# Optimization experiments

Measured on AMD Instinct MI355X. Metric: run time of the kernel, lower is better.

## Reference

```python
import jax, jax.numpy as jnp
import numpy as np

B, T, M, P = 128, 256, 256, 256  # batch, time, encoder dim m, decoder LSTM dim p


def setup_inputs() -> dict:
    key = jax.random.key(0)
    ks = jax.random.split(key, 10)
    init = lambda k, shape: (jax.random.normal(k, shape, jnp.float32) * 0.05)
    return {
        "data": jax.random.normal(ks[0], (B, T - 1, 1), jnp.float32),
        "enc_h": jax.random.normal(ks[1], (B, T, M), jnp.float32),
        "h0": jnp.zeros((B, P), jnp.float32),
        "c0": jnp.zeros((B, P), jnp.float32),
        # Dense(1) on concat([x_t, context]) -> input dim 1 + M
        "Wd": init(ks[2], (1 + M, 1)), "bd": jnp.zeros((1,), jnp.float32),
        # LSTM(p): kernel (in=1, 4p), recurrent (p, 4p), bias (4p); gate order i,f,g,o (keras)
        "Wk": init(ks[3], (1, 4 * P)), "Wr": init(ks[4], (P, 4 * P)),
        "bl": jnp.zeros((4 * P,), jnp.float32),
        # TemporalAttention: w1: m->m, w2: 2p->m, v: m->1
        "W1": init(ks[5], (M, M)), "b1": jnp.zeros((M,), jnp.float32),
        "W2": init(ks[6], (2 * P, M)), "b2": jnp.zeros((M,), jnp.float32),
        "Wv": init(ks[7], (M, 1)), "bv": jnp.zeros((1,), jnp.float32),
    }


def reference(data, enc_h, h0, c0, Wd, bd, Wk, Wr, bl, W1, b1, W2, b2, Wv, bv):
    # w1(enc_h) is loop-invariant: precompute once (same math as per-step recompute)
    pre = enc_h @ W1 + b1  # (B, T, M)
    ctx0 = jnp.zeros((enc_h.shape[0], enc_h.shape[2]), enc_h.dtype)  # (B, M)

    def step(carry, x_t):
        h, c, ctx = carry  # (B,P), (B,P), (B,M)
        # x_tilde = Dense(1)(concat([x_t, context]))
        xin = jnp.concatenate([x_t, ctx], axis=-1) @ Wd + bd  # (B, 1)
        # keras LSTM cell, gate order i, f, g, o
        z = xin @ Wk + h @ Wr + bl  # (B, 4P)
        i, f, g, o = jnp.split(z, 4, axis=-1)
        c_new = jax.nn.sigmoid(f) * c + jax.nn.sigmoid(i) * jnp.tanh(g)
        h_new = jax.nn.sigmoid(o) * jnp.tanh(c_new)
        # temporal attention over encoder states
        q = jnp.concatenate([h_new, c_new], axis=-1) @ W2 + b2  # (B, M)
        score = jnp.tanh(pre + q[:, None, :]) @ Wv + bv  # (B, T, 1)
        beta = jax.nn.softmax(score[..., 0], axis=1)  # (B, T)
        ctx_new = jnp.einsum('bt,btm->bm', beta, enc_h)  # (B, M)
        return (h_new, c_new, ctx_new), None

    xs = jnp.swapaxes(data, 0, 1)  # (T-1, B, 1)
    (h, c, ctx), _ = jax.lax.scan(jax.checkpoint(step), (h0, c0, ctx0), xs)
    # concat([h_s[:, None, :], context_v], axis=-1) -> (B, 1, P + M)
    return jnp.concatenate([h, ctx], axis=-1)[:, None, :]
```

## Files before the change

kernel.cpp:

```cpp
#include <hip/hip_runtime.h>
#include <hip/hip_fp16.h>

#define NB 128
#define TT 256
#define MM 256
#define PP 256
#define QSCALE 2.8853900817779268f

typedef unsigned int uint;
typedef _Float16 hf2 __attribute__((ext_vector_type(2)));

__device__ __forceinline__ float dot2f(uint a, uint b, float c){
#if defined(__AMDGCN__) && __has_builtin(__builtin_amdgcn_fdot2)
    return __builtin_amdgcn_fdot2(__builtin_bit_cast(hf2, a), __builtin_bit_cast(hf2, b), c, false);
#else
    float2 fa = __half22float2(__builtin_bit_cast(__half2, a));
    float2 fb = __half22float2(__builtin_bit_cast(__half2, b));
    return fmaf(fa.x, fb.x, fmaf(fa.y, fb.y, c));
#endif
}

__device__ __forceinline__ float frcp(float x){ return __builtin_amdgcn_rcpf(x); }
#if defined(__AMDGCN__) && __has_builtin(__builtin_amdgcn_exp2f)
__device__ __forceinline__ float fexp2(float x){ return __builtin_amdgcn_exp2f(x); }
#else
__device__ __forceinline__ float fexp2(float x){ return exp2f(x); }
#endif
__device__ __forceinline__ float fsig(float x){ return frcp(1.f + __expf(-x)); }
__device__ __forceinline__ float ftanh(float x){ return fmaf(-2.f, frcp(1.f + __expf(2.f*x)), 1.f); }

__device__ __forceinline__ float term2(uint ep, uint eq, uint wv, float acc){
    hf2 d = __builtin_bit_cast(hf2, ep) * __builtin_bit_cast(hf2, eq)
          + hf2{(_Float16)1.f, (_Float16)1.f};
    const __half2 r = h2rcp(__builtin_bit_cast(__half2, d));
    return dot2f(__builtin_bit_cast(uint, r), wv, acc);
}

__device__ __forceinline__ float wsum(float v){
    #pragma unroll
    for(int o=32;o;o>>=1) v += __shfl_xor(v,o);
    return v;
}

__global__ __launch_bounds__(256) void prep_pre(
    const float* __restrict__ enc, const float* __restrict__ W1,
    const float* __restrict__ b1, __half* __restrict__ preE)
{
    const int row0 = blockIdx.x * 32;
    const int col  = threadIdx.x;
    float acc[32];
    const float bias = b1[col];
    #pragma unroll
    for (int r=0;r<32;++r) acc[r]=bias;
    for (int k=0;k<256;k+=4){
        const float w0 = W1[(size_t)(k+0)*256+col];
        const float w1 = W1[(size_t)(k+1)*256+col];
        const float w2 = W1[(size_t)(k+2)*256+col];
        const float w3 = W1[(size_t)(k+3)*256+col];
        #pragma unroll
        for (int r=0;r<32;++r){
            const float4 e = *(const float4*)(enc + (size_t)(row0+r)*256 + k);
            acc[r] = fmaf(e.x,w0, fmaf(e.y,w1, fmaf(e.z,w2, fmaf(e.w,w3, acc[r]))));
        }
    }
    #pragma unroll
    for (int r=0;r<32;++r) preE[(size_t)(row0+r)*256+col] = __float2half(fexp2(acc[r]*QSCALE));
}

__global__ __launch_bounds__(256) void pack_wr4(const float* __restrict__ Wr, uint4* __restrict__ Wp){
    const int idx = blockIdx.x*256 + threadIdx.x;
    const int k4 = idx >> 9, j2 = idx & 511;
    const int k = 4*k4, j = 2*j2;
    const __half2 x = __floats2half2_rn(Wr[(size_t)(k+0)*1024+j],   Wr[(size_t)(k+1)*1024+j]);
    const __half2 y = __floats2half2_rn(Wr[(size_t)(k+2)*1024+j],   Wr[(size_t)(k+3)*1024+j]);
    const __half2 z = __floats2half2_rn(Wr[(size_t)(k+0)*1024+j+1], Wr[(size_t)(k+1)*1024+j+1]);
    const __half2 w = __floats2half2_rn(Wr[(size_t)(k+2)*1024+j+1], Wr[(size_t)(k+3)*1024+j+1]);
    Wp[idx] = make_uint4(__builtin_bit_cast(uint,x), __builtin_bit_cast(uint,y),
                         __builtin_bit_cast(uint,z), __builtin_bit_cast(uint,w));
}
__global__ __launch_bounds__(256) void pack_w2q(const float* __restrict__ W2, uint4* __restrict__ Wq){
    const int idx = blockIdx.x*256 + threadIdx.x;
    const int k8 = idx >> 9, sub = (idx >> 8) & 1, m = idx & 255;
    uint o[4];
    #pragma unroll
    for (int j=0;j<4;++j){
        const int gk2 = sub*128 + k8*4 + j;
        o[j] = __builtin_bit_cast(uint, __floats2half2_rn(
            W2[(size_t)(2*gk2)*256 + m]*QSCALE, W2[(size_t)(2*gk2+1)*256 + m]*QSCALE));
    }
    Wq[idx] = make_uint4(o[0],o[1],o[2],o[3]);
}
__global__ __launch_bounds__(256) void prep_edot(
    const float* __restrict__ enc, const float* __restrict__ Wd, float* __restrict__ edot)
{
    const int row  = blockIdx.x*4 + (threadIdx.x>>6);
    const int lane = threadIdx.x & 63;
    const float4 e = *(const float4*)(enc + (size_t)row*256 + lane*4);
    float s = e.x*Wd[1+lane*4] + e.y*Wd[2+lane*4] + e.z*Wd[3+lane*4] + e.w*Wd[4+lane*4];
    s = wsum(s);
    if (lane==0) edot[row] = s;
}

__global__ __launch_bounds__(1024) void decoder_kernel(
    const float* __restrict__ data, const float* __restrict__ enc,
    const float* __restrict__ h0, const float* __restrict__ c0,
    const float* __restrict__ Wd, const float* __restrict__ bd,
    const float* __restrict__ Wk, const float* __restrict__ bl,
    const float* __restrict__ b2, const float* __restrict__ Wv,
    const float* __restrict__ bv,
    const uint4* __restrict__ Wr4,
    const uint4* __restrict__ W2q,
    const __half* __restrict__ preE,
    const float* __restrict__ edot,
    float* __restrict__ out)
{
    __shared__ __half s_pre[TT*MM];
    __shared__ float s_red[2048];
    __shared__ float s_z[1024];
    __shared__ alignas(16) __half s_hh[PP];
    __shared__ alignas(16) __half s_ch[PP];
    __shared__ float s_h[PP], s_c[PP], s_score[TT];
    __shared__ float s_r2[32];
    __shared__ __half s_Wk[1024];
    __shared__ float s_bl[1024], s_b2[MM];
    __shared__ alignas(16) uint s_eqh[128];
    __shared__ alignas(16) uint s_wvh[128];
    __shared__ float s_edot[TT], s_data[TT];
    __shared__ float s_sc2[4];

    const int tid  = threadIdx.x;
    const int lane = tid & 63;
    const int wid  = tid >> 6;
    const int b    = blockIdx.x;

    s_Wk[tid] = __float2half(Wk[tid]);
    s_bl[tid] = bl[tid];
    if (tid < MM){
        s_b2[tid] = b2[tid]*QSCALE;
        const float h0v = h0[(size_t)b*PP+tid];
        const float c0v = c0[(size_t)b*PP+tid];
        s_h[tid]  = h0v;  s_hh[tid] = __float2half(h0v);
        s_c[tid]  = c0v;  s_ch[tid] = __float2half(c0v);
        s_edot[tid] = edot[(size_t)b*TT + tid];
    }
    if (tid < TT-1) s_data[tid] = data[(size_t)b*(TT-1)+tid];
    if (tid < 16) s_r2[tid] = (tid==0) ? 1.f : 0.f;
    if (tid < 128){
        const float2 w2 = *(const float2*)(Wv + 2*tid);
        s_wvh[tid] = __builtin_bit_cast(uint, __floats2half2_rn(w2.x, w2.y));
    }
    if (tid == 0){ s_sc2[0] = bd[0]; s_sc2[2] = Wd[0]; }
    if (tid < 64){
        const float4 w4 = *(const float4*)(Wv + 4*tid);
        float s = (w4.x+w4.y)+(w4.z+w4.w);
        s = wsum(s);
        if (tid==0) s_sc2[3] = (bv[0] + s) * (0.5f*QSCALE);
    }
    __syncthreads();

    const int p = tid - 512;
    const uint4* wc = Wr4 + ((tid >= 512) ? p : 0);
    const uint2* hu2 = (const uint2*)s_hh;

    if (tid < 512){
        const uint4* g = (const uint4*)(preE + (size_t)b*TT*MM);
        const int t0 = tid >> 1, cg = (tid & 1) * 16;
        const int rsw = (t0 & 15) << 4;
        #pragma unroll
        for (int i=0;i<16;++i){
            const int c = cg + i;
            *(uint4*)((char*)s_pre + t0*512 + ((c*16) ^ rsw)) = g[t0*32 + c];
        }
    } else {
        float a0=0.f,a1=0.f,a2=0.f,a3=0.f;
        #pragma unroll 8
        for (int k=0;k<64;++k){
            const uint4 w = wc[(size_t)k*512];
            const uint2 hp = hu2[k];
            a0=dot2f(w.x,hp.x,a0); a1=dot2f(w.y,hp.y,a1);
            a2=dot2f(w.z,hp.x,a2); a3=dot2f(w.w,hp.y,a3);
        }
        *(float2*)&s_z[2*p] = make_float2(a0+a1, a2+a3);
    }
    __syncthreads();

    const float* erow_b = enc + (size_t)b*TT*MM;
    const int mq  = tid & 63;
    const int kc2 = tid >> 6;
    const int qm  = tid >> 1;
    const int qs  = tid & 1;
    const int ttx = tid >> 1;
    const int sub = tid & 1;

    for (int t=0; t<TT-1; ++t){
        float a0=0.f,a1=0.f,a2=0.f,a3=0.f;

        if (tid < PP){
            const float den = ((s_r2[0]+s_r2[1])+(s_r2[2]+s_r2[3]))
                            + ((s_r2[4]+s_r2[5])+(s_r2[6]+s_r2[7]));
            const float num = ((s_r2[8]+s_r2[9])+(s_r2[10]+s_r2[11]))
                            + ((s_r2[12]+s_r2[13])+(s_r2[14]+s_r2[15]));
            const float xin = num*frcp(den) + s_data[t]*s_sc2[2] + s_sc2[0];
            float z[4];
            #pragma unroll
            for (int g=0; g<4; ++g){
                const int j = tid + 256*g;
                z[g] = s_z[j] + xin*__half2float(s_Wk[j]) + s_bl[j];
            }
            const float gi = fsig(z[0]);
            const float gf = fsig(z[1]);
            const float gg = ftanh(z[2]);
            const float go = fsig(z[3]);
            const float c_new = gf*s_c[tid] + gi*gg;
            const float h_new = go*ftanh(c_new);
            s_c[tid] = c_new;
            s_h[tid] = h_new;
            s_hh[tid] = __float2half(h_new);
            s_ch[tid] = __float2half(c_new);
        }
        __syncthreads();

        if (tid < 512){
            float q0=0.f,q1=0.f,q2=0.f,q3=0.f;
            const uint4* wp = W2q + qs*256 + qm;
            const uint4* hb4 = qs ? (const uint4*)s_ch : (const uint4*)s_hh;
            #pragma unroll 8
            for (int k8=0;k8<32;++k8){
                const uint4 w  = wp[(size_t)k8*512];
                const uint4 h4 = hb4[k8];
                q0=dot2f(w.x,h4.x,q0); q1=dot2f(w.y,h4.y,q1);
                q2=dot2f(w.z,h4.z,q2); q3=dot2f(w.w,h4.w,q3);
            }
            float qh = (q0+q1)+(q2+q3);
            const float qfull = qh + __shfl_xor(qh,1) + s_b2[qm];
            const uint eu = (uint)__half_as_ushort(__float2half(fexp2(qfull)));
            const uint hi = __shfl_down(eu, 2);
            if ((tid & 3) == 0) s_eqh[tid>>2] = eu | (hi<<16);
        } else {
            #pragma unroll 5
            for (int k=0;k<20;++k){
                const uint4 w = wc[(size_t)k*512];
                const uint2 hp = hu2[k];
                a0=dot2f(w.x,hp.x,a0); a1=dot2f(w.y,hp.y,a1);
                a2=dot2f(w.z,hp.x,a2); a3=dot2f(w.w,hp.y,a3);
            }
        }
        __syncthreads();

        if (tid < 512){
            float sacc0=0.f, sacc1=0.f;
            const char* prow = (const char*)s_pre + ttx*512;
            const int rsw = (ttx&15)<<4;
            #pragma unroll
            for (int cch=0; cch<16; ++cch){
                const int cc = cch*2 + sub;
                const uint4 pv = *(const uint4*)(prow + ((cc*16) ^ rsw));
                const uint4 eq = *(const uint4*)&s_eqh[cc*4];
                const uint4 wv = *(const uint4*)&s_wvh[cc*4];
                sacc0 = term2(pv.x, eq.x, wv.x, sacc0);
                sacc1 = term2(pv.y, eq.y, wv.y, sacc1);
                sacc0 = term2(pv.z, eq.z, wv.z, sacc0);
                sacc1 = term2(pv.w, eq.w, wv.w, sacc1);
            }
            float sacc = sacc0 + sacc1;
            sacc += __shfl_xor(sacc, 1);
            float e = 0.f;
            if (sub == 0){
                e = fexp2(fmaf(-QSCALE, sacc, s_sc2[3]));
                s_score[ttx] = e;
            }
            float se = e, sp = e * s_edot[ttx];
            #pragma unroll
            for (int o=32;o;o>>=1){
                const float t1 = __shfl_xor(se,o);
                const float t2 = __shfl_xor(sp,o);
                se += t1; sp += t2;
            }
            if (lane==0){ s_r2[wid] = se; s_r2[8+wid] = sp; }
        } else {
            #pragma unroll 8
            for (int k=20;k<64;++k){
                const uint4 w = wc[(size_t)k*512];
                const uint2 hp = hu2[k];
                a0=dot2f(w.x,hp.x,a0); a1=dot2f(w.y,hp.y,a1);
                a2=dot2f(w.z,hp.x,a2); a3=dot2f(w.w,hp.y,a3);
            }
            *(float2*)&s_z[2*p] = make_float2(a0+a1, a2+a3);
        }
        __syncthreads();
    }

    if (tid < 512){
        float4 ca = make_float4(0.f,0.f,0.f,0.f);
        const float* ep = erow_b + (size_t)(kc2*32)*MM + mq*4;
        #pragma unroll 4
        for (int k=0;k<32;++k){
            const float bt = s_score[kc2*32+k];
            const float4 e = *(const float4*)(ep);
            ca.x = fmaf(bt,e.x,ca.x); ca.y = fmaf(bt,e.y,ca.y);
            ca.z = fmaf(bt,e.z,ca.z); ca.w = fmaf(bt,e.w,ca.w);
            ep += MM;
        }
        *(float4*)&s_red[kc2*256 + mq*4] = ca;
    }
    __syncthreads();
    if (tid < MM){
        const float den = ((s_r2[0]+s_r2[1])+(s_r2[2]+s_r2[3]))
                        + ((s_r2[4]+s_r2[5])+(s_r2[6]+s_r2[7]));
        const float rd = frcp(den);
        float s = 0.f;
        #pragma unroll
        for (int i=0;i<8;++i) s += s_red[i*256+tid];
        out[(size_t)b*512 + 256 + tid] = s*rd;
        out[(size_t)b*512 + tid]       = s_h[tid];
    }
}

extern "C" void kernel_launch(void* const* d_in, const int* in_sizes, int n_in,
                              void* d_out, int out_size, void* d_ws, size_t ws_size,
                              hipStream_t stream) {
    const float* data = (const float*)d_in[0];
    const float* enc  = (const float*)d_in[1];
    const float* h0   = (const float*)d_in[2];
    const float* c0   = (const float*)d_in[3];
    const float* Wd   = (const float*)d_in[4];
    const float* bd   = (const float*)d_in[5];
    const float* Wk   = (const float*)d_in[6];
    const float* Wr   = (const float*)d_in[7];
    const float* bl   = (const float*)d_in[8];
    const float* W1   = (const float*)d_in[9];
    const float* b1   = (const float*)d_in[10];
    const float* W2   = (const float*)d_in[11];
    const float* b2   = (const float*)d_in[12];
    const float* Wv   = (const float*)d_in[13];
    const float* bv   = (const float*)d_in[14];
    float* outp = (float*)d_out;

    char* ws = (char*)d_ws;
    __half* preE = (__half*)(ws);
    uint4*  Wr4  = (uint4*)(ws + 16777216);
    uint4*  W2q  = (uint4*)(ws + 17301504);
    float*  edot = (float*)(ws + 17563648);

    prep_pre<<<dim3((NB*TT)/32), dim3(256), 0, stream>>>(enc, W1, b1, preE);
    pack_wr4<<<dim3(128), dim3(256), 0, stream>>>(Wr, Wr4);
    pack_w2q<<<dim3(64), dim3(256), 0, stream>>>(W2, W2q);
    prep_edot<<<dim3((NB*TT)/4), dim3(256), 0, stream>>>(enc, Wd, edot);
    decoder_kernel<<<dim3(NB), dim3(1024), 0, stream>>>(
        data, enc, h0, c0, Wd, bd, Wk, bl, b2, Wv, bv,
        Wr4, W2q, preE, edot, outp);
}
```

Measured before the change: 2.582 ms.

## Spread recurrent, query and score work evenly across all 1024 threads

Before, threads split into two roles: 512 handled the query projection and attention scores, and 512 did the recurrent Wr matvec with two output columns each. Now every thread computes one Wr gate column over 8-element packed halves, does a quarter of a W2 query column, and scores a quarter of a time row. The Wr matvec chunks are interleaved with the query and score phases to hide load latency. This removes idle imbalance between the two halves, but adds more shuffles per step and doubles the number of reduction slots.

```diff
diff --git a/kernel.cpp b/kernel.cpp
--- a/kernel.cpp
+++ b/kernel.cpp
@@ -67,14 +67,14 @@
     for (int r=0;r<32;++r) preE[(size_t)(row0+r)*256+col] = __float2half(fexp2(acc[r]*QSCALE));
 }
 
-__global__ __launch_bounds__(256) void pack_wr4(const float* __restrict__ Wr, uint4* __restrict__ Wp){
+__global__ __launch_bounds__(256) void pack_wr8(const float* __restrict__ Wr, uint4* __restrict__ Wp){
     const int idx = blockIdx.x*256 + threadIdx.x;
-    const int k4 = idx >> 9, j2 = idx & 511;
-    const int k = 4*k4, j = 2*j2;
-    const __half2 x = __floats2half2_rn(Wr[(size_t)(k+0)*1024+j],   Wr[(size_t)(k+1)*1024+j]);
-    const __half2 y = __floats2half2_rn(Wr[(size_t)(k+2)*1024+j],   Wr[(size_t)(k+3)*1024+j]);
-    const __half2 z = __floats2half2_rn(Wr[(size_t)(k+0)*1024+j+1], Wr[(size_t)(k+1)*1024+j+1]);
-    const __half2 w = __floats2half2_rn(Wr[(size_t)(k+2)*1024+j+1], Wr[(size_t)(k+3)*1024+j+1]);
+    const int k8 = idx >> 10, j = idx & 1023;
+    const int k = 8*k8;
+    const __half2 x = __floats2half2_rn(Wr[(size_t)(k+0)*1024+j], Wr[(size_t)(k+1)*1024+j]);
+    const __half2 y = __floats2half2_rn(Wr[(size_t)(k+2)*1024+j], Wr[(size_t)(k+3)*1024+j]);
+    const __half2 z = __floats2half2_rn(Wr[(size_t)(k+4)*1024+j], Wr[(size_t)(k+5)*1024+j]);
+    const __half2 w = __floats2half2_rn(Wr[(size_t)(k+6)*1024+j], Wr[(size_t)(k+7)*1024+j]);
     Wp[idx] = make_uint4(__builtin_bit_cast(uint,x), __builtin_bit_cast(uint,y),
                          __builtin_bit_cast(uint,z), __builtin_bit_cast(uint,w));
 }
@@ -108,7 +108,7 @@
     const float* __restrict__ Wk, const float* __restrict__ bl,
     const float* __restrict__ b2, const float* __restrict__ Wv,
     const float* __restrict__ bv,
-    const uint4* __restrict__ Wr4,
+    const uint4* __restrict__ Wr8,
     const uint4* __restrict__ W2q,
     const __half* __restrict__ preE,
     const float* __restrict__ edot,
@@ -144,7 +144,7 @@
         s_edot[tid] = edot[(size_t)b*TT + tid];
     }
     if (tid < TT-1) s_data[tid] = data[(size_t)b*(TT-1)+tid];
-    if (tid < 16) s_r2[tid] = (tid==0) ? 1.f : 0.f;
+    if (tid < 32) s_r2[tid] = (tid==0) ? 1.f : 0.f;
     if (tid < 128){
         const float2 w2 = *(const float2*)(Wv + 2*tid);
         s_wvh[tid] = __builtin_bit_cast(uint, __floats2half2_rn(w2.x, w2.y));
@@ -158,48 +158,48 @@
     }
     __syncthreads();
 
-    const int p = tid - 512;
-    const uint4* wc = Wr4 + ((tid >= 512) ? p : 0);
-    const uint2* hu2 = (const uint2*)s_hh;
-
-    if (tid < 512){
+    const uint4* wcol = Wr8 + tid;
+    const uint4* hu4  = (const uint4*)s_hh;
+
+    const int qm    = tid >> 2;
+    const int qtr   = tid & 3;
+    const int qsub  = qtr & 1;
+    const int k8b   = (qtr >> 1) * 16;
+    const int ttx   = tid >> 2;
+    const int s4    = tid & 3;
+    const int mq    = tid & 63;
+    const int kc2   = tid >> 6;
+
+    {
         const uint4* g = (const uint4*)(preE + (size_t)b*TT*MM);
-        const int t0 = tid >> 1, cg = (tid & 1) * 16;
-        const int rsw = (t0 & 15) << 4;
+        const int t0 = tid >> 2, c0i = (tid & 3) * 8;
+        const int rs = (t0 & 15) << 1;
         #pragma unroll
-        for (int i=0;i<16;++i){
-            const int c = cg + i;
-            *(uint4*)((char*)s_pre + t0*512 + ((c*16) ^ rsw)) = g[t0*32 + c];
-        }
-    } else {
+        for (int i=0;i<8;++i){
+            const int c = c0i + i;
+            *(uint4*)((char*)s_pre + t0*512 + ((c ^ rs)<<4)) = g[t0*32 + c];
+        }
         float a0=0.f,a1=0.f,a2=0.f,a3=0.f;
         #pragma unroll 8
-        for (int k=0;k<64;++k){
-            const uint4 w = wc[(size_t)k*512];
-            const uint2 hp = hu2[k];
-            a0=dot2f(w.x,hp.x,a0); a1=dot2f(w.y,hp.y,a1);
-            a2=dot2f(w.z,hp.x,a2); a3=dot2f(w.w,hp.y,a3);
-        }
-        *(float2*)&s_z[2*p] = make_float2(a0+a1, a2+a3);
+        for (int k8=0;k8<32;++k8){
+            const uint4 w = wcol[(size_t)k8*1024];
+            const uint4 h4 = hu4[k8];
+            a0=dot2f(w.x,h4.x,a0); a1=dot2f(w.y,h4.y,a1);
+            a2=dot2f(w.z,h4.z,a2); a3=dot2f(w.w,h4.w,a3);
+        }
+        s_z[tid] = (a0+a1)+(a2+a3);
     }
     __syncthreads();
 
     const float* erow_b = enc + (size_t)b*TT*MM;
-    const int mq  = tid & 63;
-    const int kc2 = tid >> 6;
-    const int qm  = tid >> 1;
-    const int qs  = tid & 1;
-    const int ttx = tid >> 1;
-    const int sub = tid & 1;
 
     for (int t=0; t<TT-1; ++t){
         float a0=0.f,a1=0.f,a2=0.f,a3=0.f;
 
         if (tid < PP){
-            const float den = ((s_r2[0]+s_r2[1])+(s_r2[2]+s_r2[3]))
-                            + ((s_r2[4]+s_r2[5])+(s_r2[6]+s_r2[7]));
-            const float num = ((s_r2[8]+s_r2[9])+(s_r2[10]+s_r2[11]))
-                            + ((s_r2[12]+s_r2[13])+(s_r2[14]+s_r2[15]));
+            float den = 0.f, num = 0.f;
+            #pragma unroll
+            for (int i=0;i<16;++i){ den += s_r2[i]; num += s_r2[16+i]; }
             const float xin = num*frcp(den) + s_data[t]*s_sc2[2] + s_sc2[0];
             float z[4];
             #pragma unroll
@@ -220,41 +220,50 @@
         }
         __syncthreads();
 
-        if (tid < 512){
+        {
+            #pragma unroll
+            for (int k8=0;k8<8;++k8){
+                const uint4 w = wcol[(size_t)k8*1024];
+                const uint4 h4 = hu4[k8];
+                a0=dot2f(w.x,h4.x,a0); a1=dot2f(w.y,h4.y,a1);
+                a2=dot2f(w.z,h4.z,a2); a3=dot2f(w.w,h4.w,a3);
+            }
             float q0=0.f,q1=0.f,q2=0.f,q3=0.f;
-            const uint4* wp = W2q + qs*256 + qm;
-            const uint4* hb4 = qs ? (const uint4*)s_ch : (const uint4*)s_hh;
+            const uint4* wp = W2q + (size_t)k8b*512 + qsub*256 + qm;
+            const uint4* hb4 = qsub ? (const uint4*)s_ch : (const uint4*)s_hh;
             #pragma unroll 8
-            for (int k8=0;k8<32;++k8){
-                const uint4 w  = wp[(size_t)k8*512];
-                const uint4 h4 = hb4[k8];
+            for (int kk=0;kk<16;++kk){
+                const uint4 w  = wp[(size_t)kk*512];
+                const uint4 h4 = hb4[k8b + kk];
                 q0=dot2f(w.x,h4.x,q0); q1=dot2f(w.y,h4.y,q1);
                 q2=dot2f(w.z,h4.z,q2); q3=dot2f(w.w,h4.w,q3);
             }
             float qh = (q0+q1)+(q2+q3);
-            const float qfull = qh + __shfl_xor(qh,1) + s_b2[qm];
+            qh += __shfl_xor(qh,1);
+            qh += __shfl_xor(qh,2);
+            const float qfull = qh + s_b2[qm];
             const uint eu = (uint)__half_as_ushort(__float2half(fexp2(qfull)));
-            const uint hi = __shfl_down(eu, 2);
-            if ((tid & 3) == 0) s_eqh[tid>>2] = eu | (hi<<16);
-        } else {
-            #pragma unroll 5
-            for (int k=0;k<20;++k){
-                const uint4 w = wc[(size_t)k*512];
-                const uint2 hp = hu2[k];
-                a0=dot2f(w.x,hp.x,a0); a1=dot2f(w.y,hp.y,a1);
-                a2=dot2f(w.z,hp.x,a2); a3=dot2f(w.w,hp.y,a3);
-            }
+            const uint hi = __shfl_down(eu, 4);
+            if ((tid & 7) == 0) s_eqh[tid>>3] = (eu & 0xffffu) | (hi<<16);
         }
         __syncthreads();
 
-        if (tid < 512){
+        {
             float sacc0=0.f, sacc1=0.f;
             const char* prow = (const char*)s_pre + ttx*512;
-            const int rsw = (ttx&15)<<4;
-            #pragma unroll
-            for (int cch=0; cch<16; ++cch){
-                const int cc = cch*2 + sub;
-                const uint4 pv = *(const uint4*)(prow + ((cc*16) ^ rsw));
+            const int rs = (ttx & 15) << 1;
+            #pragma unroll
+            for (int i=0;i<8;++i){
+                #pragma unroll
+                for (int u=0;u<3;++u){
+                    const int k8 = 8 + i*3 + u;
+                    const uint4 w = wcol[(size_t)k8*1024];
+                    const uint4 h4 = hu4[k8];
+                    a0=dot2f(w.x,h4.x,a0); a1=dot2f(w.y,h4.y,a1);
+                    a2=dot2f(w.z,h4.z,a2); a3=dot2f(w.w,h4.w,a3);
+                }
+                const int cc = i*4 + s4;
+                const uint4 pv = *(const uint4*)(prow + ((cc ^ rs)<<4));
                 const uint4 eq = *(const uint4*)&s_eqh[cc*4];
                 const uint4 wv = *(const uint4*)&s_wvh[cc*4];
                 sacc0 = term2(pv.x, eq.x, wv.x, sacc0);
@@ -262,30 +271,24 @@
                 sacc0 = term2(pv.z, eq.z, wv.z, sacc0);
                 sacc1 = term2(pv.w, eq.w, wv.w, sacc1);
             }
+            s_z[tid] = (a0+a1)+(a2+a3);
             float sacc = sacc0 + sacc1;
-            sacc += __shfl_xor(sacc, 1);
-            float e = 0.f;
-            if (sub == 0){
+            sacc += __shfl_xor(sacc,1);
+            sacc += __shfl_xor(sacc,2);
+            float e = 0.f, sp = 0.f;
+            if (s4 == 0){
                 e = fexp2(fmaf(-QSCALE, sacc, s_sc2[3]));
                 s_score[ttx] = e;
-            }
-            float se = e, sp = e * s_edot[ttx];
+                sp = e * s_edot[ttx];
+            }
+            float se = e;
             #pragma unroll
             for (int o=32;o;o>>=1){
                 const float t1 = __shfl_xor(se,o);
                 const float t2 = __shfl_xor(sp,o);
                 se += t1; sp += t2;
             }
-            if (lane==0){ s_r2[wid] = se; s_r2[8+wid] = sp; }
-        } else {
-            #pragma unroll 8
-            for (int k=20;k<64;++k){
-                const uint4 w = wc[(size_t)k*512];
-                const uint2 hp = hu2[k];
-                a0=dot2f(w.x,hp.x,a0); a1=dot2f(w.y,hp.y,a1);
-                a2=dot2f(w.z,hp.x,a2); a3=dot2f(w.w,hp.y,a3);
-            }
-            *(float2*)&s_z[2*p] = make_float2(a0+a1, a2+a3);
+            if (lane==0){ s_r2[wid] = se; s_r2[16+wid] = sp; }
         }
         __syncthreads();
     }
@@ -305,8 +308,9 @@
     }
     __syncthreads();
     if (tid < MM){
-        const float den = ((s_r2[0]+s_r2[1])+(s_r2[2]+s_r2[3]))
-                        + ((s_r2[4]+s_r2[5])+(s_r2[6]+s_r2[7]));
+        float den = 0.f;
+        #pragma unroll
+        for (int i=0;i<16;++i) den += s_r2[i];
         const float rd = frcp(den);
         float s = 0.f;
         #pragma unroll
@@ -338,15 +342,15 @@
 
     char* ws = (char*)d_ws;
     __half* preE = (__half*)(ws);
-    uint4*  Wr4  = (uint4*)(ws + 16777216);
+    uint4*  Wr8  = (uint4*)(ws + 16777216);
     uint4*  W2q  = (uint4*)(ws + 17301504);
     float*  edot = (float*)(ws + 17563648);
 
     prep_pre<<<dim3((NB*TT)/32), dim3(256), 0, stream>>>(enc, W1, b1, preE);
-    pack_wr4<<<dim3(128), dim3(256), 0, stream>>>(Wr, Wr4);
+    pack_wr8<<<dim3(128), dim3(256), 0, stream>>>(Wr, Wr8);
     pack_w2q<<<dim3(64), dim3(256), 0, stream>>>(W2, W2q);
     prep_edot<<<dim3((NB*TT)/4), dim3(256), 0, stream>>>(enc, Wd, edot);
     decoder_kernel<<<dim3(NB), dim3(1024), 0, stream>>>(
         data, enc, h0, c0, Wd, bd, Wk, bl, b2, Wv, bv,
-        Wr4, W2q, preE, edot, outp);
-}
+        Wr8, W2q, preE, edot, outp);
+}
```

New measurement: 7.132 ms. 2.76x slower.
